# Kernel tuning notes

Measured on AMD Instinct MI355X. Metric: run time of the kernel, lower is better.

The kernel has to match this reference:

```python
import jax, jax.numpy as jnp
import numpy as np

N = 50000
E = 1600000
D_IN = 512   # embedding_num - 1
D_OUT = 512  # output1_dim


def setup_inputs() -> dict:
    key = jax.random.key(0)
    ks = jax.random.split(key, 16)
    A1_tensor = jax.random.normal(ks[0], (N, D_IN + 1), dtype=jnp.float32)
    adj_rows = jax.random.randint(ks[1], (E,), 0, N, dtype=jnp.int32)
    adj_cols = jax.random.randint(ks[2], (E,), 0, N, dtype=jnp.int32)
    adj_vals = jax.random.uniform(ks[3], (E,), dtype=jnp.float32)
    s = 1.0 / np.sqrt(D_IN)
    Lin1 = jax.random.uniform(ks[4], (D_IN, D_OUT), minval=-s, maxval=s, dtype=jnp.float32)
    Lin1_bias = jax.random.uniform(ks[5], (D_OUT,), minval=-s, maxval=s, dtype=jnp.float32)
    n = jax.random.uniform(ks[6], (N, 1), minval=0.0, maxval=1.0, dtype=jnp.float32)
    W1 = jax.random.uniform(ks[7], (D_IN, D_OUT), minval=-s, maxval=s, dtype=jnp.float32)
    b1 = jax.random.uniform(ks[8], (D_OUT,), minval=-s, maxval=s, dtype=jnp.float32)
    s2 = 1.0 / np.sqrt(D_OUT)
    W2 = jax.random.uniform(ks[9], (D_OUT, D_OUT), minval=-s2, maxval=s2, dtype=jnp.float32)
    b2 = jax.random.uniform(ks[10], (D_OUT,), minval=-s2, maxval=s2, dtype=jnp.float32)
    W3 = jax.random.uniform(ks[11], (D_OUT, D_OUT), minval=-s2, maxval=s2, dtype=jnp.float32)
    b3 = jax.random.uniform(ks[12], (D_OUT,), minval=-s2, maxval=s2, dtype=jnp.float32)
    return {"A1_tensor": A1_tensor, "adj_rows": adj_rows, "adj_cols": adj_cols,
            "adj_vals": adj_vals, "Lin1": Lin1, "Lin1_bias": Lin1_bias, "n": n,
            "W1": W1, "b1": b1, "W2": W2, "b2": b2, "W3": W3, "b3": b3}


def reference(A1_tensor, adj_rows, adj_cols, adj_vals, Lin1, Lin1_bias, n,
              W1, b1, W2, b2, W3, b3):
    num_nodes = A1_tensor.shape[0]

    def spmm(h):  # sparse adj @ h via edge-list gather + segment_sum
        return jax.ops.segment_sum(adj_vals[:, None] * h[adj_cols], adj_rows,
                                   num_segments=num_nodes)

    x = A1_tensor[:, 1:]                      # drop first feature column (dropout = identity at eval)
    a0 = x @ Lin1 + Lin1_bias                 # [N, D_OUT]
    a1 = a0 * n
    x1 = spmm(x @ W1 + b1)                    # gc1
    x1 = a1 + x1 * (1.0 - n)                  # gated blend
    x2 = spmm(x1 @ W2 + b2)                   # gc2
    x2 = spmm(x2 @ W3 + b3)                   # gc3
    return jnp.concatenate([x2, a0], axis=-1) # [N, 2*D_OUT]
```

## Files before the change

kernel.cpp:

```cpp
#include <hip/hip_runtime.h>
#include <stdint.h>

#define DD 512

typedef __bf16 bf16x8 __attribute__((ext_vector_type(8)));
typedef float f32x4 __attribute__((ext_vector_type(4)));

__device__ __forceinline__ unsigned short f2bf(float f) {
  uint32_t u = __builtin_bit_cast(uint32_t, f);
  u += 0x7fff + ((u >> 16) & 1);
  return (unsigned short)(u >> 16);
}
__device__ __forceinline__ float bfbits2f(uint32_t lo16) {
  return __builtin_bit_cast(float, lo16 << 16);
}

__global__ void hist_kernel(const int* __restrict__ rows, int* __restrict__ counts, int E) {
  int i = blockIdx.x * blockDim.x + threadIdx.x;
  if (i < E) atomicAdd(&counts[rows[i]], 1);
}

__global__ __launch_bounds__(256) void scan_block(const int* __restrict__ counts,
                                                  int* __restrict__ offs, int* __restrict__ bsum,
                                                  int n) {
  __shared__ int sm[256];
  int t = threadIdx.x;
  int i = blockIdx.x * 256 + t;
  int v = (i < n) ? counts[i] : 0;
  sm[t] = v;
  __syncthreads();
  for (int o = 1; o < 256; o <<= 1) {
    int x = (t >= o) ? sm[t - o] : 0;
    __syncthreads();
    sm[t] += x;
    __syncthreads();
  }
  if (i < n) offs[i + 1] = sm[t];
  if (t == 255) bsum[blockIdx.x] = sm[255];
}

__global__ __launch_bounds__(256) void scan_tops(int* __restrict__ bsum, int nb) {
  __shared__ int sm[256];
  int t = threadIdx.x;
  int v = (t < nb) ? bsum[t] : 0;
  sm[t] = v;
  __syncthreads();
  for (int o = 1; o < 256; o <<= 1) {
    int x = (t >= o) ? sm[t - o] : 0;
    __syncthreads();
    sm[t] += x;
    __syncthreads();
  }
  if (t < nb) bsum[t] = sm[t];
}

__global__ __launch_bounds__(256) void scan_add(int* __restrict__ offs,
                                                const int* __restrict__ bsum, int n) {
  int i = blockIdx.x * 256 + threadIdx.x;
  int add = (blockIdx.x > 0) ? bsum[blockIdx.x - 1] : 0;
  if (i < n) offs[i + 1] += add;
  if (i == 0) offs[0] = 0;
}

__global__ void scatter_kernel(const int* __restrict__ rows, const int* __restrict__ colsIn,
                               const float* __restrict__ valsIn, const int* __restrict__ offs,
                               int* __restrict__ cursor, int* __restrict__ colsC,
                               unsigned short* __restrict__ valsC, int E) {
  int i = blockIdx.x * blockDim.x + threadIdx.x;
  if (i < E) {
    int r = rows[i];
    int p = offs[r] + atomicAdd(&cursor[r], 1);
    colsC[p] = colsIn[i];
    valsC[p] = f2bf(valsIn[i]);
  }
}

__global__ __launch_bounds__(256) void convert_x(const float* __restrict__ A1,
                                                 __bf16* __restrict__ Xb, int N) {
  int id = blockIdx.x * 256 + threadIdx.x;
  int total = (N * DD) >> 3;
  if (id >= total) return;
  int r = id >> 6;
  int c = (id & 63) * 8;
  const float* p = A1 + (size_t)r * 513 + 1 + c;
  unsigned short h[8];
#pragma unroll
  for (int k = 0; k < 8; ++k) h[k] = f2bf(p[k]);
  uint4 o;
  o.x = (uint32_t)h[0] | ((uint32_t)h[1] << 16);
  o.y = (uint32_t)h[2] | ((uint32_t)h[3] << 16);
  o.z = (uint32_t)h[4] | ((uint32_t)h[5] << 16);
  o.w = (uint32_t)h[6] | ((uint32_t)h[7] << 16);
  *(uint4*)(Xb + (size_t)r * DD + c) = o;
}

__global__ __launch_bounds__(256) void convert_wt(const float* __restrict__ W,
                                                  __bf16* __restrict__ Wt) {
  __shared__ float tile[32][33];
  int bx = blockIdx.x * 32;
  int by = blockIdx.y * 32;
  int tx = threadIdx.x & 31, ty = threadIdx.x >> 5;
#pragma unroll
  for (int q = 0; q < 4; ++q)
    tile[ty + q * 8][tx] = W[(size_t)(by + ty + q * 8) * DD + bx + tx];
  __syncthreads();
  unsigned short* Wts = (unsigned short*)Wt;
#pragma unroll
  for (int q = 0; q < 4; ++q)
    Wts[(size_t)(bx + ty + q * 8) * DD + by + tx] = f2bf(tile[tx][ty + q * 8]);
}

template <int MODE>
__global__ __launch_bounds__(256) void gemm_mfma(
    const __bf16* __restrict__ A,
    const __bf16* __restrict__ Bt,
    const float* __restrict__ bias,
    __bf16* __restrict__ Yb,
    float* __restrict__ out,
    const float* __restrict__ nvec,
    int M) {
  __shared__ __bf16 As[128][72];
  __shared__ __bf16 Bs[128][72];
  const int tid = threadIdx.x;
  const int bm = blockIdx.x * 128;
  const int bn = blockIdx.y * 128;
  const int lane = tid & 63;
  const int w = tid >> 6;
  const int wm = (w & 1) * 64;
  const int wn = (w >> 1) * 64;
  const int m16 = lane & 15;
  const int quad = lane >> 4;

  f32x4 acc[4][4];
#pragma unroll
  for (int i = 0; i < 4; ++i)
#pragma unroll
    for (int j = 0; j < 4; ++j) acc[i][j] = (f32x4){0.f, 0.f, 0.f, 0.f};

  for (int k0 = 0; k0 < DD; k0 += 64) {
#pragma unroll
    for (int l = 0; l < 4; ++l) {
      int id = tid + l * 256;
      int row = id >> 3;
      int ck = (id & 7) * 8;
      int gm = bm + row;
      if (gm >= M) gm = M - 1;
      *(uint4*)&As[row][ck] = *(const uint4*)(A + (size_t)gm * DD + k0 + ck);
      *(uint4*)&Bs[row][ck] = *(const uint4*)(Bt + (size_t)(bn + row) * DD + k0 + ck);
    }
    __syncthreads();
#pragma unroll
    for (int ks = 0; ks < 2; ++ks) {
      int kb = ks * 32 + quad * 8;
      bf16x8 af[4], bf[4];
#pragma unroll
      for (int i = 0; i < 4; ++i) af[i] = *(const bf16x8*)&As[wm + i * 16 + m16][kb];
#pragma unroll
      for (int j = 0; j < 4; ++j) bf[j] = *(const bf16x8*)&Bs[wn + j * 16 + m16][kb];
#pragma unroll
      for (int i = 0; i < 4; ++i)
#pragma unroll
        for (int j = 0; j < 4; ++j)
          acc[i][j] = __builtin_amdgcn_mfma_f32_16x16x32_bf16(af[i], bf[j], acc[i][j], 0, 0, 0);
    }
    __syncthreads();
  }

  float bv[4];
#pragma unroll
  for (int j = 0; j < 4; ++j) bv[j] = bias[bn + wn + j * 16 + m16];

  unsigned short* Ybs = (unsigned short*)Yb;
#pragma unroll
  for (int i = 0; i < 4; ++i) {
#pragma unroll
    for (int r = 0; r < 4; ++r) {
      int row = bm + wm + i * 16 + quad * 4 + r;
      if (row < M) {
        if (MODE == 0) {
          float nv = nvec[row];
#pragma unroll
          for (int j = 0; j < 4; ++j) {
            int c = bn + wn + j * 16 + m16;
            float a0 = acc[i][j][r] + bv[j];
            out[(size_t)row * 1024 + 512 + c] = a0;
            out[(size_t)row * 1024 + c] = a0 * nv;
          }
        } else {
#pragma unroll
          for (int j = 0; j < 4; ++j) {
            int c = bn + wn + j * 16 + m16;
            Ybs[(size_t)row * DD + c] = f2bf(acc[i][j][r] + bv[j]);
          }
        }
      }
    }
  }
}

template <int MODE>
__global__ __launch_bounds__(256) void spmm_bf16(
    const int* __restrict__ offs, const int* __restrict__ cols,
    const unsigned short* __restrict__ vals,
    const __bf16* __restrict__ H,
    __bf16* __restrict__ Xb, float* __restrict__ outF,
    const float* __restrict__ a1, const float* __restrict__ nvec) {
  int r = blockIdx.x;
  int t = threadIdx.x;
  int s = offs[r], e = offs[r + 1];
  int d = t * 2;
  float acc0 = 0.f, acc1 = 0.f;
  int i = s;
  for (; i + 4 <= e; i += 4) {
    int c0 = cols[i], c1 = cols[i + 1], c2 = cols[i + 2], c3 = cols[i + 3];
    float v0 = bfbits2f(vals[i]);
    float v1 = bfbits2f(vals[i + 1]);
    float v2 = bfbits2f(vals[i + 2]);
    float v3 = bfbits2f(vals[i + 3]);
    uint32_t h0 = *(const uint32_t*)(H + (size_t)c0 * DD + d);
    uint32_t h1 = *(const uint32_t*)(H + (size_t)c1 * DD + d);
    uint32_t h2 = *(const uint32_t*)(H + (size_t)c2 * DD + d);
    uint32_t h3 = *(const uint32_t*)(H + (size_t)c3 * DD + d);
    acc0 += v0 * bfbits2f(h0 & 0xffffu) + v1 * bfbits2f(h1 & 0xffffu) +
            v2 * bfbits2f(h2 & 0xffffu) + v3 * bfbits2f(h3 & 0xffffu);
    acc1 += v0 * bfbits2f(h0 >> 16) + v1 * bfbits2f(h1 >> 16) +
            v2 * bfbits2f(h2 >> 16) + v3 * bfbits2f(h3 >> 16);
  }
  for (; i < e; ++i) {
    int c = cols[i];
    float v = bfbits2f(vals[i]);
    uint32_t h = *(const uint32_t*)(H + (size_t)c * DD + d);
    acc0 += v * bfbits2f(h & 0xffffu);
    acc1 += v * bfbits2f(h >> 16);
  }
  if (MODE == 2) {
    float2 o;
    o.x = acc0;
    o.y = acc1;
    *(float2*)(outF + (size_t)r * 1024 + d) = o;
  } else {
    if (MODE == 1) {
      float g = 1.f - nvec[r];
      float2 a = *(const float2*)(a1 + (size_t)r * 1024 + d);
      acc0 = a.x + acc0 * g;
      acc1 = a.y + acc1 * g;
    }
    uint32_t p = ((uint32_t)f2bf(acc1) << 16) | (uint32_t)f2bf(acc0);
    *(uint32_t*)((unsigned short*)Xb + (size_t)r * DD + d) = p;
  }
}

extern "C" void kernel_launch(void* const* d_in, const int* in_sizes, int n_in,
                              void* d_out, int out_size, void* d_ws, size_t ws_size,
                              hipStream_t stream) {
  const float* A1       = (const float*)d_in[0];
  const int*   adj_rows = (const int*)d_in[1];
  const int*   adj_cols = (const int*)d_in[2];
  const float* adj_vals = (const float*)d_in[3];
  const float* Lin1     = (const float*)d_in[4];
  const float* Lin1b    = (const float*)d_in[5];
  const float* nvec     = (const float*)d_in[6];
  const float* W1       = (const float*)d_in[7];
  const float* b1       = (const float*)d_in[8];
  const float* W2       = (const float*)d_in[9];
  const float* b2       = (const float*)d_in[10];
  const float* W3       = (const float*)d_in[11];
  const float* b3       = (const float*)d_in[12];
  const int N = in_sizes[6];
  const int E = in_sizes[1];
  float* out = (float*)d_out;

  uint8_t* base = (uint8_t*)d_ws;
  size_t off = 0;
  auto take = [&](size_t bytes) -> void* {
    off = (off + 255) & ~(size_t)255;
    void* r = base + off;
    off += bytes;
    return r;
  };
  __bf16* Xb     = (__bf16*)take((size_t)N * DD * 2);
  __bf16* Yb     = (__bf16*)take((size_t)N * DD * 2);
  __bf16* Wt     = (__bf16*)take((size_t)4 * DD * DD * 2);
  int*    colsC  = (int*)take((size_t)E * sizeof(int));
  unsigned short* valsC = (unsigned short*)take((size_t)E * 2);
  int*    offs   = (int*)take((size_t)(N + 1) * sizeof(int));
  int*    counts = (int*)take((size_t)N * sizeof(int));
  int*    bsum   = (int*)take(1024);
  (void)ws_size; (void)n_in; (void)out_size;

  __bf16* Wt0 = Wt;
  __bf16* Wt1 = Wt + (size_t)DD * DD;
  __bf16* Wt2 = Wt + (size_t)2 * DD * DD;
  __bf16* Wt3 = Wt + (size_t)3 * DD * DD;

  int eb = (E + 255) / 256;
  int nb = (N + 255) / 256;

  hipMemsetAsync(counts, 0, (size_t)N * sizeof(int), stream);
  hist_kernel<<<eb, 256, 0, stream>>>(adj_rows, counts, E);
  scan_block<<<nb, 256, 0, stream>>>(counts, offs, bsum, N);
  scan_tops<<<1, 256, 0, stream>>>(bsum, nb);
  scan_add<<<nb, 256, 0, stream>>>(offs, bsum, N);
  hipMemsetAsync(counts, 0, (size_t)N * sizeof(int), stream);
  scatter_kernel<<<eb, 256, 0, stream>>>(adj_rows, adj_cols, adj_vals, offs, counts,
                                         colsC, valsC, E);

  convert_x<<<(N * DD / 8 + 255) / 256, 256, 0, stream>>>(A1, Xb, N);
  dim3 wgrid(16, 16);
  convert_wt<<<wgrid, 256, 0, stream>>>(Lin1, Wt0);
  convert_wt<<<wgrid, 256, 0, stream>>>(W1, Wt1);
  convert_wt<<<wgrid, 256, 0, stream>>>(W2, Wt2);
  convert_wt<<<wgrid, 256, 0, stream>>>(W3, Wt3);

  dim3 ggrid((N + 127) / 128, 4);
  gemm_mfma<0><<<ggrid, 256, 0, stream>>>(Xb, Wt0, Lin1b, nullptr, out, nvec, N);
  gemm_mfma<1><<<ggrid, 256, 0, stream>>>(Xb, Wt1, b1, Yb, nullptr, nullptr, N);
  spmm_bf16<1><<<N, 256, 0, stream>>>(offs, colsC, valsC, Yb, Xb, nullptr, out, nvec);
  gemm_mfma<1><<<ggrid, 256, 0, stream>>>(Xb, Wt2, b2, Yb, nullptr, nullptr, N);
  spmm_bf16<0><<<N, 256, 0, stream>>>(offs, colsC, valsC, Yb, Xb, nullptr, nullptr, nullptr);
  gemm_mfma<1><<<ggrid, 256, 0, stream>>>(Xb, Wt3, b3, Yb, nullptr, nullptr, N);
  spmm_bf16<2><<<N, 256, 0, stream>>>(offs, colsC, valsC, Yb, nullptr, out, nullptr, nullptr);
}
```

Before: 1.352 ms.

## Store GEMM output in 32-column slices and slice SpMM for cache locality

The GEMM epilogue now writes its bf16 output in a column-sliced layout: 16 slices of 32 columns, each contiguous across all rows. The SpMM kernel is restructured so each block handles 16 rows for one slice, with blocks ordered so eight slices run together in each half of the grid. The goal is a smaller working set of gathered H rows per slice so random neighbor gathers hit L2/MALL more often. The cost is that each gather is only 64 bytes per row, and cols/vals are re-read once per slice (16x more index traffic).

```diff
diff --git a/kernel.cpp b/kernel.cpp
--- a/kernel.cpp
+++ b/kernel.cpp
@@ -171,6 +171,7 @@
   for (int j = 0; j < 4; ++j) bv[j] = bias[bn + wn + j * 16 + m16];
 
   unsigned short* Ybs = (unsigned short*)Yb;
+  const size_t sliceStride = (size_t)M * 32;
 #pragma unroll
   for (int i = 0; i < 4; ++i) {
 #pragma unroll
@@ -190,7 +191,8 @@
 #pragma unroll
           for (int j = 0; j < 4; ++j) {
             int c = bn + wn + j * 16 + m16;
-            Ybs[(size_t)row * DD + c] = f2bf(acc[i][j][r] + bv[j]);
+            Ybs[(size_t)(c >> 5) * sliceStride + (size_t)row * 32 + (c & 31)] =
+                f2bf(acc[i][j][r] + bv[j]);
           }
         }
       }
@@ -199,16 +201,27 @@
 }
 
 template <int MODE>
-__global__ __launch_bounds__(256) void spmm_bf16(
+__global__ __launch_bounds__(256) void spmm_sliced(
     const int* __restrict__ offs, const int* __restrict__ cols,
     const unsigned short* __restrict__ vals,
     const __bf16* __restrict__ H,
     __bf16* __restrict__ Xb, float* __restrict__ outF,
-    const float* __restrict__ a1, const float* __restrict__ nvec) {
-  int r = blockIdx.x;
-  int t = threadIdx.x;
+    const float* __restrict__ a1, const float* __restrict__ nvec, int N) {
+  const int RB = (N + 15) >> 4;
+  const int HALF = RB * 8;
+  int b = blockIdx.x;
+  int half = (b >= HALF) ? 1 : 0;
+  int idx = b - half * HALF;
+  int slice = half * 8 + (idx & 7);
+  int rowblk = idx >> 3;
+  int g = threadIdx.x >> 4;
+  int l = threadIdx.x & 15;
+  int r = rowblk * 16 + g;
+  if (r >= N) return;
+
+  const unsigned short* Hs =
+      (const unsigned short*)H + (size_t)slice * N * 32 + (size_t)l * 2;
   int s = offs[r], e = offs[r + 1];
-  int d = t * 2;
   float acc0 = 0.f, acc1 = 0.f;
   int i = s;
   for (; i + 4 <= e; i += 4) {
@@ -217,10 +230,10 @@
     float v1 = bfbits2f(vals[i + 1]);
     float v2 = bfbits2f(vals[i + 2]);
     float v3 = bfbits2f(vals[i + 3]);
-    uint32_t h0 = *(const uint32_t*)(H + (size_t)c0 * DD + d);
-    uint32_t h1 = *(const uint32_t*)(H + (size_t)c1 * DD + d);
-    uint32_t h2 = *(const uint32_t*)(H + (size_t)c2 * DD + d);
-    uint32_t h3 = *(const uint32_t*)(H + (size_t)c3 * DD + d);
+    uint32_t h0 = *(const uint32_t*)(Hs + (size_t)c0 * 32);
+    uint32_t h1 = *(const uint32_t*)(Hs + (size_t)c1 * 32);
+    uint32_t h2 = *(const uint32_t*)(Hs + (size_t)c2 * 32);
+    uint32_t h3 = *(const uint32_t*)(Hs + (size_t)c3 * 32);
     acc0 += v0 * bfbits2f(h0 & 0xffffu) + v1 * bfbits2f(h1 & 0xffffu) +
             v2 * bfbits2f(h2 & 0xffffu) + v3 * bfbits2f(h3 & 0xffffu);
     acc1 += v0 * bfbits2f(h0 >> 16) + v1 * bfbits2f(h1 >> 16) +
@@ -229,10 +242,12 @@
   for (; i < e; ++i) {
     int c = cols[i];
     float v = bfbits2f(vals[i]);
-    uint32_t h = *(const uint32_t*)(H + (size_t)c * DD + d);
+    uint32_t h = *(const uint32_t*)(Hs + (size_t)c * 32);
     acc0 += v * bfbits2f(h & 0xffffu);
     acc1 += v * bfbits2f(h >> 16);
   }
+
+  int d = slice * 32 + l * 2;
   if (MODE == 2) {
     float2 o;
     o.x = acc0;
@@ -240,10 +255,10 @@
     *(float2*)(outF + (size_t)r * 1024 + d) = o;
   } else {
     if (MODE == 1) {
-      float g = 1.f - nvec[r];
+      float gq = 1.f - nvec[r];
       float2 a = *(const float2*)(a1 + (size_t)r * 1024 + d);
-      acc0 = a.x + acc0 * g;
-      acc1 = a.y + acc1 * g;
+      acc0 = a.x + acc0 * gq;
+      acc1 = a.y + acc1 * gq;
     }
     uint32_t p = ((uint32_t)f2bf(acc1) << 16) | (uint32_t)f2bf(acc0);
     *(uint32_t*)((unsigned short*)Xb + (size_t)r * DD + d) = p;
@@ -313,11 +328,14 @@
   convert_wt<<<wgrid, 256, 0, stream>>>(W3, Wt3);
 
   dim3 ggrid((N + 127) / 128, 4);
+  int RB = (N + 15) / 16;
+  int sgrid = RB * 16;
+
   gemm_mfma<0><<<ggrid, 256, 0, stream>>>(Xb, Wt0, Lin1b, nullptr, out, nvec, N);
   gemm_mfma<1><<<ggrid, 256, 0, stream>>>(Xb, Wt1, b1, Yb, nullptr, nullptr, N);
-  spmm_bf16<1><<<N, 256, 0, stream>>>(offs, colsC, valsC, Yb, Xb, nullptr, out, nvec);
+  spmm_sliced<1><<<sgrid, 256, 0, stream>>>(offs, colsC, valsC, Yb, Xb, nullptr, out, nvec, N);
   gemm_mfma<1><<<ggrid, 256, 0, stream>>>(Xb, Wt2, b2, Yb, nullptr, nullptr, N);
-  spmm_bf16<0><<<N, 256, 0, stream>>>(offs, colsC, valsC, Yb, Xb, nullptr, nullptr, nullptr);
+  spmm_sliced<0><<<sgrid, 256, 0, stream>>>(offs, colsC, valsC, Yb, Xb, nullptr, nullptr, nullptr, N);
   gemm_mfma<1><<<ggrid, 256, 0, stream>>>(Xb, Wt3, b3, Yb, nullptr, nullptr, N);
-  spmm_bf16<2><<<N, 256, 0, stream>>>(offs, colsC, valsC, Yb, nullptr, out, nullptr, nullptr);
-}
+  spmm_sliced<2><<<sgrid, 256, 0, stream>>>(offs, colsC, valsC, Yb, nullptr, out, nullptr, nullptr, N);
+}
```

Result: slower. 1.493 ms (+10.5%).
